# Optimization experiments

Measured on AMD Instinct MI355X. Metric: run time of the kernel, lower is better.

## Reference

```python
import jax, jax.numpy as jnp
import numpy as np

N = 50000   # nodes
E = 1600000 # edges
D = 64      # feature dim


def gcn_conv(x, edge_index, W, b):
    """PyG GCNConv: x' = D^-1/2 (A+I) D^-1/2 (x W) + b."""
    n = x.shape[0]
    xw = x @ W                                   # [N, D_out] linear first (PyG order)
    loop = jnp.arange(n)
    src = jnp.concatenate([edge_index[0], loop])  # add self-loops
    dst = jnp.concatenate([edge_index[1], loop])
    deg = jax.ops.segment_sum(jnp.ones_like(src, dtype=xw.dtype), dst, num_segments=n)
    dinv = jnp.where(deg > 0, jax.lax.rsqrt(deg), 0.0)
    norm = dinv[src] * dinv[dst]                  # symmetric normalization
    out = jax.ops.segment_sum(norm[:, None] * xw[src], dst, num_segments=n)
    return out + b


def setup_inputs() -> dict:
    key = jax.random.key(0)
    k1, k2, k3, k4 = jax.random.split(key, 4)
    x = jax.random.normal(k1, (N, D), dtype=jnp.float32)
    edge_index = jax.random.randint(k2, (2, E), 0, N, dtype=jnp.int64)
    s = 1.0 / np.sqrt(D)
    W1 = jax.random.normal(k3, (D, D), dtype=jnp.float32) * s
    b1 = jnp.zeros((D,), dtype=jnp.float32)
    W2 = jax.random.normal(k4, (D, D), dtype=jnp.float32) * s
    b2 = jnp.zeros((D,), dtype=jnp.float32)
    return {"x": x, "edge_index": edge_index, "W1": W1, "b1": b1, "W2": W2, "b2": b2}


def reference(x, edge_index, W1, b1, W2, b2):
    h = gcn_conv(x, edge_index, W1, b1)
    h = jax.nn.relu(h)  # dropout is identity in eval mode
    out = gcn_conv(h, edge_index, W2, b2)
    return out
```

## Files before the change

### kernel.cpp

```cpp
#include <hip/hip_runtime.h>
#include <hip/hip_fp16.h>


#define P1_EDGES 4096
#define BSTRIDE 16384

typedef float vfloat4 __attribute__((ext_vector_type(4)));

__global__ void bucket_kernel(const int* __restrict__ src, const int* __restrict__ dst,
                              unsigned* __restrict__ cursor, unsigned* __restrict__ ebuf,
                              int e, int B) {
    __shared__ unsigned hist[256];
    __shared__ unsigned base[256];
    for (int i = threadIdx.x; i < B; i += 1024) hist[i] = 0;
    __syncthreads();
    int e0 = blockIdx.x * P1_EDGES;
    int tbase = e0 + (int)threadIdx.x * 4;
    int4 sv = make_int4(0, 0, 0, 0), dv = make_int4(0, 0, 0, 0);
    if (tbase + 3 < e) {
        sv = ((const int4*)(src + e0))[threadIdx.x];
        dv = ((const int4*)(dst + e0))[threadIdx.x];
    } else {
        if (tbase + 0 < e) { sv.x = src[tbase + 0]; dv.x = dst[tbase + 0]; }
        if (tbase + 1 < e) { sv.y = src[tbase + 1]; dv.y = dst[tbase + 1]; }
        if (tbase + 2 < e) { sv.z = src[tbase + 2]; dv.z = dst[tbase + 2]; }
    }
    unsigned bk[4], rk[4], pk[4];
    bool vk[4];
#pragma unroll
    for (int k = 0; k < 4; ++k) {
        int t = tbase + k;
        vk[k] = (t < e);
        bk[k] = 0; rk[k] = 0; pk[k] = 0;
        if (vk[k]) {
            unsigned s = (unsigned)(k == 0 ? sv.x : k == 1 ? sv.y : k == 2 ? sv.z : sv.w);
            unsigned d = (unsigned)(k == 0 ? dv.x : k == 1 ? dv.y : k == 2 ? dv.z : dv.w);
            unsigned b = d >> 8;
            bk[k] = b;
            rk[k] = atomicAdd(&hist[b], 1u);
            pk[k] = (d << 16) | s;
        }
    }
    __syncthreads();
    for (int i = threadIdx.x; i < B; i += 1024)
        base[i] = hist[i] ? atomicAdd(&cursor[i], hist[i]) : 0u;
    __syncthreads();
#pragma unroll
    for (int k = 0; k < 4; ++k)
        if (vk[k]) {
            unsigned slot = base[bk[k]] + rk[k];
            if (slot < (unsigned)BSTRIDE)
                ebuf[(size_t)bk[k] * BSTRIDE + slot] = pk[k];
        }
}

__global__ void statsfill_kernel(const unsigned* __restrict__ ebuf,
                                 const unsigned* __restrict__ bcnt,
                                 unsigned* __restrict__ rpf, float* __restrict__ dinv,
                                 unsigned short* __restrict__ csr, int n, int e) {
    __shared__ unsigned pos[256];
    __shared__ unsigned sh[256];
    __shared__ unsigned rpl[256];
    __shared__ unsigned bs;
    int b = blockIdx.x;
    int w0 = b << 8;
    int wlen = min(w0 + 256, n) - w0;
    unsigned c0 = 0;
    if (threadIdx.x < 256) { c0 = bcnt[threadIdx.x]; sh[threadIdx.x] = c0; }
    __syncthreads();
    for (int off = 1; off < 256; off <<= 1) {
        unsigned t = 0;
        if (threadIdx.x < 256 && threadIdx.x >= (unsigned)off) t = sh[threadIdx.x - off];
        __syncthreads();
        if (threadIdx.x < 256) sh[threadIdx.x] += t;
        __syncthreads();
    }
    if (threadIdx.x == (unsigned)b) bs = sh[b] - c0;
    if (threadIdx.x < 256) pos[threadIdx.x] = 0;
    __syncthreads();
    unsigned cnt = bcnt[b];
    const unsigned* eb = ebuf + (size_t)b * BSTRIDE;
    for (unsigned j = threadIdx.x; j < cnt; j += 1024)
        atomicAdd(&pos[(eb[j] >> 16) - w0], 1u);
    __syncthreads();
    unsigned v = 0;
    if (threadIdx.x < 256) { v = pos[threadIdx.x]; sh[threadIdx.x] = v; }
    __syncthreads();
    for (int off = 1; off < 256; off <<= 1) {
        unsigned t = 0;
        if (threadIdx.x < 256 && threadIdx.x >= (unsigned)off) t = sh[threadIdx.x - off];
        __syncthreads();
        if (threadIdx.x < 256) sh[threadIdx.x] += t;
        __syncthreads();
    }
    if (threadIdx.x < 256) {
        unsigned rp = bs + sh[threadIdx.x] - v;
        rpl[threadIdx.x] = rp;
        if ((int)threadIdx.x < wlen) {
            rpf[w0 + threadIdx.x] = rp;
            dinv[w0 + threadIdx.x] = rsqrtf((float)v + 1.0f);
        }
        pos[threadIdx.x] = 0;
    }
    if (b == (int)gridDim.x - 1 && threadIdx.x == 0) rpf[n] = (unsigned)e;
    __syncthreads();
    for (unsigned j = threadIdx.x; j < cnt; j += 1024) {
        unsigned p = eb[j];
        unsigned d = (p >> 16) - w0;
        unsigned r = atomicAdd(&pos[d], 1u);
        csr[rpl[d] + r] = (unsigned short)(p & 0xffffu);
    }
}

__global__ void gemm64_kernel(const float4* __restrict__ X4, const float* __restrict__ W,
                              const float* __restrict__ dinv, __half* __restrict__ Yh, int n) {
    __shared__ float4 Ws[64][16];
    for (int i = threadIdx.x; i < 64 * 16; i += blockDim.x)
        Ws[i >> 4][i & 15] = ((const float4*)W)[i];
    __syncthreads();
    int lane = threadIdx.x & 63;
    int l = lane & 15;
    int gbase = lane & 48;
    int wid = blockIdx.x * (blockDim.x >> 6) + (threadIdx.x >> 6);
    int row = wid * 4 + (lane >> 4);
    if (row >= n) return;
    float4 xv = X4[(size_t)row * 16 + l];
    float4 acc = make_float4(0.f, 0.f, 0.f, 0.f);
#pragma unroll
    for (int k = 0; k < 64; ++k) {
        float comp = (k & 3) == 0 ? xv.x : (k & 3) == 1 ? xv.y : (k & 3) == 2 ? xv.z : xv.w;
        float a = __shfl(comp, gbase + (k >> 2));
        float4 w = Ws[k][l];
        acc.x = fmaf(a, w.x, acc.x); acc.y = fmaf(a, w.y, acc.y);
        acc.z = fmaf(a, w.z, acc.z); acc.w = fmaf(a, w.w, acc.w);
    }
    float di = dinv[row];
    __half2 h0 = __floats2half2_rn(acc.x * di, acc.y * di);
    __half2 h1 = __floats2half2_rn(acc.z * di, acc.w * di);
    uint2 o;
    o.x = *(const unsigned*)&h0;
    o.y = *(const unsigned*)&h1;
    *(uint2*)(Yh + (size_t)row * 64 + 4 * l) = o;
}

struct f8 { float4 a, b; };

__device__ __forceinline__ f8 aggregate_row8(const __half* __restrict__ xwh,
                                             const unsigned* __restrict__ csrw,
                                             unsigned start, unsigned end,
                                             int row, int l8, int gbase) {
    f8 acc;
    {
        uint4 hv = *(const uint4*)(xwh + (size_t)row * 64 + 8 * l8);
        float2 f0 = __half22float2(*(const __half2*)&hv.x);
        float2 f1 = __half22float2(*(const __half2*)&hv.y);
        float2 f2 = __half22float2(*(const __half2*)&hv.z);
        float2 f3 = __half22float2(*(const __half2*)&hv.w);
        acc.a = make_float4(f0.x, f0.y, f1.x, f1.y);
        acc.b = make_float4(f2.x, f2.y, f3.x, f3.y);
    }
    unsigned wb = start >> 1;
    unsigned jw = wb + (unsigned)l8;
    unsigned ed = (jw * 2 < end) ? __builtin_nontemporal_load(&csrw[jw]) : 0u;
    for (unsigned base = wb; base * 2 < end; base += 8) {
        unsigned jn = base + 8 + (unsigned)l8;
        unsigned ed_next = (jn * 2 < end) ? __builtin_nontemporal_load(&csrw[jn]) : 0u;
#pragma unroll
        for (int t = 0; t < 8; ++t) {
            unsigned p = __shfl(ed, gbase + t);
            unsigned i0 = (base + (unsigned)t) * 2;
            int s0 = (int)(p & 0xffffu);
            int s1 = (int)(p >> 16);
            float w0 = (i0 >= start && i0 < end) ? 1.0f : 0.0f;
            float w1 = (i0 + 1 < end) ? 1.0f : 0.0f;
            uint4 hv0 = *(const uint4*)(xwh + (size_t)s0 * 64 + 8 * l8);
            uint4 hv1 = *(const uint4*)(xwh + (size_t)s1 * 64 + 8 * l8);
            float2 a0 = __half22float2(*(const __half2*)&hv0.x);
            float2 a1 = __half22float2(*(const __half2*)&hv0.y);
            float2 a2 = __half22float2(*(const __half2*)&hv0.z);
            float2 a3 = __half22float2(*(const __half2*)&hv0.w);
            acc.a.x = fmaf(w0, a0.x, acc.a.x); acc.a.y = fmaf(w0, a0.y, acc.a.y);
            acc.a.z = fmaf(w0, a1.x, acc.a.z); acc.a.w = fmaf(w0, a1.y, acc.a.w);
            acc.b.x = fmaf(w0, a2.x, acc.b.x); acc.b.y = fmaf(w0, a2.y, acc.b.y);
            acc.b.z = fmaf(w0, a3.x, acc.b.z); acc.b.w = fmaf(w0, a3.y, acc.b.w);
            float2 c0 = __half22float2(*(const __half2*)&hv1.x);
            float2 c1 = __half22float2(*(const __half2*)&hv1.y);
            float2 c2 = __half22float2(*(const __half2*)&hv1.z);
            float2 c3 = __half22float2(*(const __half2*)&hv1.w);
            acc.a.x = fmaf(w1, c0.x, acc.a.x); acc.a.y = fmaf(w1, c0.y, acc.a.y);
            acc.a.z = fmaf(w1, c1.x, acc.a.z); acc.a.w = fmaf(w1, c1.y, acc.a.w);
            acc.b.x = fmaf(w1, c2.x, acc.b.x); acc.b.y = fmaf(w1, c2.y, acc.b.y);
            acc.b.z = fmaf(w1, c3.x, acc.b.z); acc.b.w = fmaf(w1, c3.y, acc.b.w);
        }
        ed = ed_next;
    }
    return acc;
}

__global__ void __launch_bounds__(256, 3)
gather_gemm_kernel(const __half* __restrict__ xwh, const unsigned* __restrict__ csrw,
                   const unsigned* __restrict__ row_ptr,
                   const float* __restrict__ b1, const float* __restrict__ W2,
                   __half* __restrict__ Yh, int n) {
    __shared__ float4 Ws[64][16];
    for (int i = threadIdx.x; i < 64 * 16; i += blockDim.x)
        Ws[i >> 4][i & 15] = ((const float4*)W2)[i];
    __syncthreads();
    int lane = threadIdx.x & 63;
    int l8 = lane & 7;
    int gbase = lane & 56;
    int wid = blockIdx.x * (blockDim.x >> 6) + (threadIdx.x >> 6);
    int row = wid * 8 + (lane >> 3);
    if (row >= n) return;
    unsigned start = row_ptr[row], end = row_ptr[row + 1];
    float di = rsqrtf((float)(end - start) + 1.0f);
    f8 acc = aggregate_row8(xwh, csrw, start, end, row, l8, gbase);
    float4 ba = ((const float4*)b1)[2 * l8];
    float4 bb = ((const float4*)b1)[2 * l8 + 1];
    float h0 = fmaxf(fmaf(di, acc.a.x, ba.x), 0.f);
    float h1 = fmaxf(fmaf(di, acc.a.y, ba.y), 0.f);
    float h2 = fmaxf(fmaf(di, acc.a.z, ba.z), 0.f);
    float h3 = fmaxf(fmaf(di, acc.a.w, ba.w), 0.f);
    float h4 = fmaxf(fmaf(di, acc.b.x, bb.x), 0.f);
    float h5 = fmaxf(fmaf(di, acc.b.y, bb.y), 0.f);
    float h6 = fmaxf(fmaf(di, acc.b.z, bb.z), 0.f);
    float h7 = fmaxf(fmaf(di, acc.b.w, bb.w), 0.f);
    float4 o0 = make_float4(0.f, 0.f, 0.f, 0.f);
    float4 o1 = make_float4(0.f, 0.f, 0.f, 0.f);
#pragma unroll
    for (int k = 0; k < 64; ++k) {
        float comp = (k & 7) == 0 ? h0 : (k & 7) == 1 ? h1 : (k & 7) == 2 ? h2 :
                     (k & 7) == 3 ? h3 : (k & 7) == 4 ? h4 : (k & 7) == 5 ? h5 :
                     (k & 7) == 6 ? h6 : h7;
        float a = __shfl(comp, gbase + (k >> 3));
        float4 w0 = Ws[k][2 * l8];
        float4 w1 = Ws[k][2 * l8 + 1];
        o0.x = fmaf(a, w0.x, o0.x); o0.y = fmaf(a, w0.y, o0.y);
        o0.z = fmaf(a, w0.z, o0.z); o0.w = fmaf(a, w0.w, o0.w);
        o1.x = fmaf(a, w1.x, o1.x); o1.y = fmaf(a, w1.y, o1.y);
        o1.z = fmaf(a, w1.z, o1.z); o1.w = fmaf(a, w1.w, o1.w);
    }
    __half2 p0 = __floats2half2_rn(o0.x * di, o0.y * di);
    __half2 p1 = __floats2half2_rn(o0.z * di, o0.w * di);
    __half2 p2 = __floats2half2_rn(o1.x * di, o1.y * di);
    __half2 p3 = __floats2half2_rn(o1.z * di, o1.w * di);
    uint4 o;
    o.x = *(const unsigned*)&p0; o.y = *(const unsigned*)&p1;
    o.z = *(const unsigned*)&p2; o.w = *(const unsigned*)&p3;
    *(uint4*)(Yh + (size_t)row * 64 + 8 * l8) = o;
}

__global__ void __launch_bounds__(256, 3)
gather_out_kernel(const __half* __restrict__ xwh, const unsigned* __restrict__ csrw,
                  const unsigned* __restrict__ row_ptr,
                  const float* __restrict__ bias, float4* __restrict__ out4, int n) {
    int lane = threadIdx.x & 63;
    int l8 = lane & 7;
    int gbase = lane & 56;
    int wid = blockIdx.x * (blockDim.x >> 6) + (threadIdx.x >> 6);
    int row = wid * 8 + (lane >> 3);
    if (row >= n) return;
    unsigned start = row_ptr[row], end = row_ptr[row + 1];
    float di = rsqrtf((float)(end - start) + 1.0f);
    f8 acc = aggregate_row8(xwh, csrw, start, end, row, l8, gbase);
    float4 ba = ((const float4*)bias)[2 * l8];
    float4 bb = ((const float4*)bias)[2 * l8 + 1];
    vfloat4 oa, ob;
    oa.x = fmaf(di, acc.a.x, ba.x); oa.y = fmaf(di, acc.a.y, ba.y);
    oa.z = fmaf(di, acc.a.z, ba.z); oa.w = fmaf(di, acc.a.w, ba.w);
    ob.x = fmaf(di, acc.b.x, bb.x); ob.y = fmaf(di, acc.b.y, bb.y);
    ob.z = fmaf(di, acc.b.z, bb.z); ob.w = fmaf(di, acc.b.w, bb.w);
    vfloat4* o4 = (vfloat4*)out4;
    __builtin_nontemporal_store(oa, &o4[(size_t)row * 16 + 2 * l8]);
    __builtin_nontemporal_store(ob, &o4[(size_t)row * 16 + 2 * l8 + 1]);
}

extern "C" void kernel_launch(void* const* d_in, const int* in_sizes, int n_in,
                              void* d_out, int out_size, void* d_ws, size_t ws_size,
                              hipStream_t stream) {
    const float* x  = (const float*)d_in[0];
    const int*   ei = (const int*)d_in[1];
    const float* W1 = (const float*)d_in[2];
    const float* b1 = (const float*)d_in[3];
    const float* W2 = (const float*)d_in[4];
    const float* b2 = (const float*)d_in[5];
    const int n = in_sizes[0] / 64;
    const int e = in_sizes[1] / 2;
    const int* src = ei;
    const int* dst = ei + e;

    char* ws = (char*)d_ws;
    size_t off = 0;
    auto alloc = [&](size_t bytes) -> void* {
        void* p = ws + off;
        off = (off + bytes + 255) & ~(size_t)255;
        return p;
    };
    unsigned* rpf    = (unsigned*)alloc((size_t)(n + 1) * 4);
    float*    dinv   = (float*)alloc((size_t)n * 4);
    unsigned* cursor = (unsigned*)alloc(256 * 4);
    unsigned short* csr = (unsigned short*)alloc(((size_t)e / 2 + 64) * 4);
    const int B = (n + 255) / 256;
    size_t ebuf_sz = (size_t)B * BSTRIDE * 4;
    size_t ov = ebuf_sz > (size_t)n * 64 * 2 ? ebuf_sz : (size_t)n * 64 * 2;
    char*     overlay = (char*)alloc(ov);
    unsigned* ebuf    = (unsigned*)overlay;
    __half*   xwh1    = (__half*)overlay;
    __half*   xwh2    = (__half*)alloc((size_t)n * 64 * 2);
    float*    outf    = (float*)d_out;

    const int nbP1 = (e + P1_EDGES - 1) / P1_EDGES;

    hipMemsetAsync(cursor, 0, 256 * 4, stream);
    bucket_kernel<<<nbP1, 1024, 0, stream>>>(src, dst, cursor, ebuf, e, B);
    statsfill_kernel<<<B, 1024, 0, stream>>>(ebuf, cursor, rpf, dinv, csr, n, e);

    const int gblk16 = (n + 15) / 16;
    const int gblk32 = (n + 31) / 32;

    gemm64_kernel<<<gblk16, 256, 0, stream>>>((const float4*)x, W1, dinv, xwh1, n);
    gather_gemm_kernel<<<gblk32, 256, 0, stream>>>(xwh1, (const unsigned*)csr, rpf, b1, W2, xwh2, n);

    gather_out_kernel<<<gblk32, 256, 0, stream>>>(xwh2, (const unsigned*)csr, rpf, b2, (float4*)outf, n);
}
```

Before: 175.5 us.

## Fuse first GEMM into bucket kernel and apply dinv scaling in statsfill

The layer-1 GEMM now runs as extra blocks of the edge-bucketing kernel, so it overlaps with bucketing instead of waiting for degree stats, and one launch is removed. Because dinv is not yet known at that point, the unscaled half-precision XW is stored, and statsfill rescales each row by its rsqrt degree in place. The ebuf/xwh1 overlay is dropped so both buffers can coexist, which raises workspace use. The extra read-modify-write pass over xwh1 and a second fp16 rounding are the costs.

New measurement: 171.5 us (median of 2 runs). 2.3% less time.

```diff
diff --git a/kernel.cpp b/kernel.cpp
--- a/kernel.cpp
+++ b/kernel.cpp
@@ -7,60 +7,94 @@
 
 typedef float vfloat4 __attribute__((ext_vector_type(4)));
 
-__global__ void bucket_kernel(const int* __restrict__ src, const int* __restrict__ dst,
-                              unsigned* __restrict__ cursor, unsigned* __restrict__ ebuf,
-                              int e, int B) {
+__global__ void bucket_gemm_kernel(const int* __restrict__ src, const int* __restrict__ dst,
+                                   unsigned* __restrict__ cursor, unsigned* __restrict__ ebuf,
+                                   const float4* __restrict__ X4, const float* __restrict__ W,
+                                   __half* __restrict__ Yh,
+                                   int e, int B, int n, int nbP1) {
     __shared__ unsigned hist[256];
     __shared__ unsigned base[256];
-    for (int i = threadIdx.x; i < B; i += 1024) hist[i] = 0;
-    __syncthreads();
-    int e0 = blockIdx.x * P1_EDGES;
-    int tbase = e0 + (int)threadIdx.x * 4;
-    int4 sv = make_int4(0, 0, 0, 0), dv = make_int4(0, 0, 0, 0);
-    if (tbase + 3 < e) {
-        sv = ((const int4*)(src + e0))[threadIdx.x];
-        dv = ((const int4*)(dst + e0))[threadIdx.x];
+    __shared__ float4 Ws[64][16];
+    int bid = blockIdx.x;
+    if (bid < nbP1) {
+        for (int i = threadIdx.x; i < B; i += 1024) hist[i] = 0;
+        __syncthreads();
+        int e0 = bid * P1_EDGES;
+        int tbase = e0 + (int)threadIdx.x * 4;
+        int4 sv = make_int4(0, 0, 0, 0), dv = make_int4(0, 0, 0, 0);
+        if (tbase + 3 < e) {
+            sv = ((const int4*)(src + e0))[threadIdx.x];
+            dv = ((const int4*)(dst + e0))[threadIdx.x];
+        } else {
+            if (tbase + 0 < e) { sv.x = src[tbase + 0]; dv.x = dst[tbase + 0]; }
+            if (tbase + 1 < e) { sv.y = src[tbase + 1]; dv.y = dst[tbase + 1]; }
+            if (tbase + 2 < e) { sv.z = src[tbase + 2]; dv.z = dst[tbase + 2]; }
+        }
+        unsigned bk[4], rk[4], pk[4];
+        bool vk[4];
+#pragma unroll
+        for (int k = 0; k < 4; ++k) {
+            int t = tbase + k;
+            vk[k] = (t < e);
+            bk[k] = 0; rk[k] = 0; pk[k] = 0;
+            if (vk[k]) {
+                unsigned s = (unsigned)(k == 0 ? sv.x : k == 1 ? sv.y : k == 2 ? sv.z : sv.w);
+                unsigned d = (unsigned)(k == 0 ? dv.x : k == 1 ? dv.y : k == 2 ? dv.z : dv.w);
+                unsigned b = d >> 8;
+                bk[k] = b;
+                rk[k] = atomicAdd(&hist[b], 1u);
+                pk[k] = (d << 16) | s;
+            }
+        }
+        __syncthreads();
+        for (int i = threadIdx.x; i < B; i += 1024)
+            base[i] = hist[i] ? atomicAdd(&cursor[i], hist[i]) : 0u;
+        __syncthreads();
+#pragma unroll
+        for (int k = 0; k < 4; ++k)
+            if (vk[k]) {
+                unsigned slot = base[bk[k]] + rk[k];
+                if (slot < (unsigned)BSTRIDE)
+                    ebuf[(size_t)bk[k] * BSTRIDE + slot] = pk[k];
+            }
     } else {
-        if (tbase + 0 < e) { sv.x = src[tbase + 0]; dv.x = dst[tbase + 0]; }
-        if (tbase + 1 < e) { sv.y = src[tbase + 1]; dv.y = dst[tbase + 1]; }
-        if (tbase + 2 < e) { sv.z = src[tbase + 2]; dv.z = dst[tbase + 2]; }
-    }
-    unsigned bk[4], rk[4], pk[4];
-    bool vk[4];
-#pragma unroll
-    for (int k = 0; k < 4; ++k) {
-        int t = tbase + k;
-        vk[k] = (t < e);
-        bk[k] = 0; rk[k] = 0; pk[k] = 0;
-        if (vk[k]) {
-            unsigned s = (unsigned)(k == 0 ? sv.x : k == 1 ? sv.y : k == 2 ? sv.z : sv.w);
-            unsigned d = (unsigned)(k == 0 ? dv.x : k == 1 ? dv.y : k == 2 ? dv.z : dv.w);
-            unsigned b = d >> 8;
-            bk[k] = b;
-            rk[k] = atomicAdd(&hist[b], 1u);
-            pk[k] = (d << 16) | s;
+        for (int i = threadIdx.x; i < 64 * 16; i += 1024)
+            Ws[i >> 4][i & 15] = ((const float4*)W)[i];
+        __syncthreads();
+        int lane = threadIdx.x & 63;
+        int l = lane & 15;
+        int gbase = lane & 48;
+        int wid = (bid - nbP1) * 16 + (threadIdx.x >> 6);
+        int row = wid * 4 + (lane >> 4);
+        if (row >= n) return;
+        float4 xv = X4[(size_t)row * 16 + l];
+        float4 acc = make_float4(0.f, 0.f, 0.f, 0.f);
+#pragma unroll
+        for (int k = 0; k < 64; ++k) {
+            float comp = (k & 3) == 0 ? xv.x : (k & 3) == 1 ? xv.y : (k & 3) == 2 ? xv.z : xv.w;
+            float a = __shfl(comp, gbase + (k >> 2));
+            float4 w = Ws[k][l];
+            acc.x = fmaf(a, w.x, acc.x); acc.y = fmaf(a, w.y, acc.y);
+            acc.z = fmaf(a, w.z, acc.z); acc.w = fmaf(a, w.w, acc.w);
         }
-    }
-    __syncthreads();
-    for (int i = threadIdx.x; i < B; i += 1024)
-        base[i] = hist[i] ? atomicAdd(&cursor[i], hist[i]) : 0u;
-    __syncthreads();
-#pragma unroll
-    for (int k = 0; k < 4; ++k)
-        if (vk[k]) {
-            unsigned slot = base[bk[k]] + rk[k];
-            if (slot < (unsigned)BSTRIDE)
-                ebuf[(size_t)bk[k] * BSTRIDE + slot] = pk[k];
-        }
+        __half2 h0 = __floats2half2_rn(acc.x, acc.y);
+        __half2 h1 = __floats2half2_rn(acc.z, acc.w);
+        uint2 o;
+        o.x = *(const unsigned*)&h0;
+        o.y = *(const unsigned*)&h1;
+        *(uint2*)(Yh + (size_t)row * 64 + 4 * l) = o;
+    }
 }
 
 __global__ void statsfill_kernel(const unsigned* __restrict__ ebuf,
                                  const unsigned* __restrict__ bcnt,
-                                 unsigned* __restrict__ rpf, float* __restrict__ dinv,
+                                 unsigned* __restrict__ rpf,
+                                 __half* __restrict__ xwh1,
                                  unsigned short* __restrict__ csr, int n, int e) {
     __shared__ unsigned pos[256];
     __shared__ unsigned sh[256];
     __shared__ unsigned rpl[256];
+    __shared__ float dl[256];
     __shared__ unsigned bs;
     int b = blockIdx.x;
     int w0 = b << 8;
@@ -96,51 +130,35 @@
     if (threadIdx.x < 256) {
         unsigned rp = bs + sh[threadIdx.x] - v;
         rpl[threadIdx.x] = rp;
-        if ((int)threadIdx.x < wlen) {
-            rpf[w0 + threadIdx.x] = rp;
-            dinv[w0 + threadIdx.x] = rsqrtf((float)v + 1.0f);
-        }
+        dl[threadIdx.x] = rsqrtf((float)v + 1.0f);
+        if ((int)threadIdx.x < wlen) rpf[w0 + threadIdx.x] = rp;
         pos[threadIdx.x] = 0;
     }
     if (b == (int)gridDim.x - 1 && threadIdx.x == 0) rpf[n] = (unsigned)e;
     __syncthreads();
+    for (int i = threadIdx.x; i < (wlen << 3); i += 1024) {
+        int r = i >> 3, c = i & 7;
+        float di = dl[r];
+        uint4* p16 = (uint4*)(xwh1 + ((size_t)(w0 + r) << 6)) + c;
+        uint4 hv = *p16;
+        float2 f0 = __half22float2(*(const __half2*)&hv.x);
+        float2 f1 = __half22float2(*(const __half2*)&hv.y);
+        float2 f2 = __half22float2(*(const __half2*)&hv.z);
+        float2 f3 = __half22float2(*(const __half2*)&hv.w);
+        __half2 g0 = __floats2half2_rn(f0.x * di, f0.y * di);
+        __half2 g1 = __floats2half2_rn(f1.x * di, f1.y * di);
+        __half2 g2 = __floats2half2_rn(f2.x * di, f2.y * di);
+        __half2 g3 = __floats2half2_rn(f3.x * di, f3.y * di);
+        hv.x = *(const unsigned*)&g0; hv.y = *(const unsigned*)&g1;
+        hv.z = *(const unsigned*)&g2; hv.w = *(const unsigned*)&g3;
+        *p16 = hv;
+    }
     for (unsigned j = threadIdx.x; j < cnt; j += 1024) {
         unsigned p = eb[j];
         unsigned d = (p >> 16) - w0;
         unsigned r = atomicAdd(&pos[d], 1u);
         csr[rpl[d] + r] = (unsigned short)(p & 0xffffu);
     }
-}
-
-__global__ void gemm64_kernel(const float4* __restrict__ X4, const float* __restrict__ W,
-                              const float* __restrict__ dinv, __half* __restrict__ Yh, int n) {
-    __shared__ float4 Ws[64][16];
-    for (int i = threadIdx.x; i < 64 * 16; i += blockDim.x)
-        Ws[i >> 4][i & 15] = ((const float4*)W)[i];
-    __syncthreads();
-    int lane = threadIdx.x & 63;
-    int l = lane & 15;
-    int gbase = lane & 48;
-    int wid = blockIdx.x * (blockDim.x >> 6) + (threadIdx.x >> 6);
-    int row = wid * 4 + (lane >> 4);
-    if (row >= n) return;
-    float4 xv = X4[(size_t)row * 16 + l];
-    float4 acc = make_float4(0.f, 0.f, 0.f, 0.f);
-#pragma unroll
-    for (int k = 0; k < 64; ++k) {
-        float comp = (k & 3) == 0 ? xv.x : (k & 3) == 1 ? xv.y : (k & 3) == 2 ? xv.z : xv.w;
-        float a = __shfl(comp, gbase + (k >> 2));
-        float4 w = Ws[k][l];
-        acc.x = fmaf(a, w.x, acc.x); acc.y = fmaf(a, w.y, acc.y);
-        acc.z = fmaf(a, w.z, acc.z); acc.w = fmaf(a, w.w, acc.w);
-    }
-    float di = dinv[row];
-    __half2 h0 = __floats2half2_rn(acc.x * di, acc.y * di);
-    __half2 h1 = __floats2half2_rn(acc.z * di, acc.w * di);
-    uint2 o;
-    o.x = *(const unsigned*)&h0;
-    o.y = *(const unsigned*)&h1;
-    *(uint2*)(Yh + (size_t)row * 64 + 4 * l) = o;
 }
 
 struct f8 { float4 a, b; };
@@ -297,29 +315,24 @@
         return p;
     };
     unsigned* rpf    = (unsigned*)alloc((size_t)(n + 1) * 4);
-    float*    dinv   = (float*)alloc((size_t)n * 4);
     unsigned* cursor = (unsigned*)alloc(256 * 4);
     unsigned short* csr = (unsigned short*)alloc(((size_t)e / 2 + 64) * 4);
     const int B = (n + 255) / 256;
-    size_t ebuf_sz = (size_t)B * BSTRIDE * 4;
-    size_t ov = ebuf_sz > (size_t)n * 64 * 2 ? ebuf_sz : (size_t)n * 64 * 2;
-    char*     overlay = (char*)alloc(ov);
-    unsigned* ebuf    = (unsigned*)overlay;
-    __half*   xwh1    = (__half*)overlay;
-    __half*   xwh2    = (__half*)alloc((size_t)n * 64 * 2);
-    float*    outf    = (float*)d_out;
+    unsigned* ebuf   = (unsigned*)alloc((size_t)B * BSTRIDE * 4);
+    __half*   xwh1   = (__half*)alloc((size_t)n * 64 * 2);
+    __half*   xwh2   = (__half*)alloc((size_t)n * 64 * 2);
+    float*    outf   = (float*)d_out;
 
     const int nbP1 = (e + P1_EDGES - 1) / P1_EDGES;
+    const int gblk64 = (n + 63) / 64;
 
     hipMemsetAsync(cursor, 0, 256 * 4, stream);
-    bucket_kernel<<<nbP1, 1024, 0, stream>>>(src, dst, cursor, ebuf, e, B);
-    statsfill_kernel<<<B, 1024, 0, stream>>>(ebuf, cursor, rpf, dinv, csr, n, e);
-
-    const int gblk16 = (n + 15) / 16;
+    bucket_gemm_kernel<<<nbP1 + gblk64, 1024, 0, stream>>>(
+        src, dst, cursor, ebuf, (const float4*)x, W1, xwh1, e, B, n, nbP1);
+    statsfill_kernel<<<B, 1024, 0, stream>>>(ebuf, cursor, rpf, xwh1, csr, n, e);
+
     const int gblk32 = (n + 31) / 32;
 
-    gemm64_kernel<<<gblk16, 256, 0, stream>>>((const float4*)x, W1, dinv, xwh1, n);
     gather_gemm_kernel<<<gblk32, 256, 0, stream>>>(xwh1, (const unsigned*)csr, rpf, b1, W2, xwh2, n);
-
     gather_out_kernel<<<gblk32, 256, 0, stream>>>(xwh2, (const unsigned*)csr, rpf, b2, (float4*)outf, n);
 }
```
